# Optimization experiments

Measured on AMD Instinct MI355X. Metric: run time of the kernel, lower is better.

The kernel has to match this reference:

```python
import jax, jax.numpy as jnp
import numpy as np

N_NODES = 100000
N_EDGES = 1600000
IN_CH = 128
HIDDEN = 128


def setup_inputs() -> dict:
    key = jax.random.key(0)
    ks = jax.random.split(key, 8)
    def w(k, shape, fan_in):
        return jax.random.normal(k, shape, dtype=jnp.float32) * (1.0 / np.sqrt(fan_in))
    return {
        "x": jax.random.normal(ks[0], (N_NODES, IN_CH), dtype=jnp.float32),
        "edge_index": jax.random.randint(ks[1], (2, N_EDGES), 0, N_NODES, dtype=jnp.int32),
        # SAGEConv 1: lin_l (self, with bias), lin_r (neighbor mean, no bias)
        "Wl1": w(ks[2], (HIDDEN, IN_CH), IN_CH), "bl1": jnp.zeros((HIDDEN,), jnp.float32),
        "Wr1": w(ks[3], (HIDDEN, IN_CH), IN_CH),
        # SAGEConv 2
        "Wl2": w(ks[4], (HIDDEN, HIDDEN), HIDDEN), "bl2": jnp.zeros((HIDDEN,), jnp.float32),
        "Wr2": w(ks[5], (HIDDEN, HIDDEN), HIDDEN),
        # output head Linear(hidden, 1)
        "Wo": w(ks[6], (1, HIDDEN), HIDDEN), "bo": jnp.zeros((1,), jnp.float32),
    }


def _sage(x, src, dst, Wl, bl, Wr):
    # mean-aggregate source features onto destination nodes (PyG SAGEConv default)
    msg = x[src]                                             # [E, d] gather
    agg = jax.ops.segment_sum(msg, dst, num_segments=N_NODES)  # [N, d]
    cnt = jax.ops.segment_sum(jnp.ones((src.shape[0], 1), x.dtype), dst,
                              num_segments=N_NODES)            # [N, 1]
    mean = agg / jnp.maximum(cnt, 1.0)
    return x @ Wl.T + mean @ Wr.T + bl


def reference(x, edge_index, Wl1, bl1, Wr1, Wl2, bl2, Wr2, Wo, bo):
    src, dst = edge_index[0], edge_index[1]
    h = jax.nn.relu(_sage(x, src, dst, Wl1, bl1, Wr1))
    h = jax.nn.relu(_sage(h, src, dst, Wl2, bl2, Wr2))
    return (h @ Wo.T + bo).squeeze(-1)  # [N]
```

## Files before the change

### kernel.cpp

```cpp
#include <hip/hip_runtime.h>
#include <hip/hip_fp16.h>
#include <hip/hip_fp8.h>

#define N_NODES 100000
#define N_EDGES 1600000
#define C 128

#define NB_SHIFT 10
#define NB (1 << NB_SHIFT)
#define NBKT ((N_NODES + NB - 1) >> NB_SHIFT)
#define CAP 20480
#define CPT 4096
#define STG_BLOCKS ((N_EDGES + CPT - 1) / CPT)
#define CVB 782
#define PWB 32

typedef _Float16 half8 __attribute__((ext_vector_type(8)));
typedef float f32x4 __attribute__((ext_vector_type(4)));
typedef float f32x2 __attribute__((ext_vector_type(2)));

__device__ inline void fp8x4_to_f32(unsigned w, float* f) {
#if __has_builtin(__builtin_amdgcn_cvt_pk_f32_fp8)
    f32x2 lo = __builtin_amdgcn_cvt_pk_f32_fp8((int)w, false);
    f32x2 hi = __builtin_amdgcn_cvt_pk_f32_fp8((int)w, true);
    f[0] = lo[0]; f[1] = lo[1]; f[2] = hi[0]; f[3] = hi[1];
#else
    for (int i = 0; i < 4; i++) {
        __hip_fp8_e4m3 v;
        v.__x = (unsigned char)(w >> (8 * i));
        f[i] = (float)v;
    }
#endif
}

__device__ inline unsigned f32x4_to_fp8(float a, float b, float c, float d) {
#if __has_builtin(__builtin_amdgcn_cvt_pk_fp8_f32)
    int t = __builtin_amdgcn_cvt_pk_fp8_f32(a, b, 0, false);
    t = __builtin_amdgcn_cvt_pk_fp8_f32(c, d, t, true);
    return (unsigned)t;
#else
    __hip_fp8_e4m3 fa(a), fb(b), fc(c), fd(d);
    return (unsigned)fa.__x | ((unsigned)fb.__x << 8) | ((unsigned)fc.__x << 16) |
           ((unsigned)fd.__x << 24);
#endif
}

__device__ inline unsigned f32x2_to_fp8(float a, float b) {
#if __has_builtin(__builtin_amdgcn_cvt_pk_fp8_f32)
    return (unsigned)__builtin_amdgcn_cvt_pk_fp8_f32(a, b, 0, false);
#else
    __hip_fp8_e4m3 fa(a), fb(b);
    return (unsigned)fa.__x | ((unsigned)fb.__x << 8);
#endif
}


__global__ __launch_bounds__(512) void k_fusedA(
    const float* __restrict__ x, const int* __restrict__ src,
    const int* __restrict__ dst, const float* __restrict__ Wl1,
    const float* __restrict__ Wr1, const float* __restrict__ Wl2,
    const float* __restrict__ Wr2, int* __restrict__ gcur,
    uint2* __restrict__ S, __half* __restrict__ Xh, unsigned* __restrict__ X8u,
    __half* __restrict__ Wc1, __half* __restrict__ Wc2) {
    __shared__ int hist[128], sc[128], lstart[128], gbaseL[128];
    __shared__ uint2 stg[CPT];
    const int bid = blockIdx.x;
    const int t = threadIdx.x;

    if (bid < CVB) {
        const float4* xin = (const float4*)x;
        __half2* yout = (__half2*)Xh;
#pragma unroll
        for (int i = 0; i < 8; i++) {
            int idx = bid * 4096 + i * 512 + t;
            if (idx < N_NODES * C / 4) {
                float4 v = xin[idx];
                yout[idx * 2] = __floats2half2_rn(v.x, v.y);
                yout[idx * 2 + 1] = __floats2half2_rn(v.z, v.w);
                X8u[idx] = f32x4_to_fp8(v.x, v.y, v.z, v.w);
            }
        }
        return;
    }
    if (bid < CVB + PWB) {
        int i0 = ((bid - CVB) * 512 + t) * 4;
#pragma unroll
        for (int m = 0; m < 4; m++) {
            int i = i0 + m;
            if (i < 2 * 128 * 256) {
                int set = i >> 15;
                int j = i & 32767;
                int n_ = j >> 8, k = j & 255;
                const float* Wl = set ? Wl2 : Wl1;
                const float* Wr = set ? Wr2 : Wr1;
                float v = (k < 128) ? Wl[n_ * 128 + k] : Wr[n_ * 128 + (k - 128)];
                (set ? Wc2 : Wc1)[j] = __float2half_rn(v);
            }
        }
        return;
    }

    int base = (bid - CVB - PWB) * CPT;
    int cnt = N_EDGES - base;
    if (cnt > CPT) cnt = CPT;
    if (t < 128) hist[t] = 0;
    __syncthreads();
    unsigned s_[8], d_[8];
    int r_[8], b_[8];
#pragma unroll
    for (int i = 0; i < 8; i++) {
        int li = i * 512 + t;
        if (li < cnt) {
            int e = base + li;
            s_[i] = src[e];
            d_[i] = dst[e];
            b_[i] = d_[i] >> NB_SHIFT;
            r_[i] = atomicAdd(&hist[b_[i]], 1);
        } else {
            r_[i] = -1;
        }
    }
    __syncthreads();
    int hv = (t < 128) ? hist[t] : 0;
    if (t < 128) sc[t] = hv;
    __syncthreads();
    for (int off = 1; off < 128; off <<= 1) {
        int u = (t < 128 && t >= off) ? sc[t - off] : 0;
        __syncthreads();
        if (t < 128) sc[t] += u;
        __syncthreads();
    }
    if (t < 128) lstart[t] = sc[t] - hv;
    if (t < NBKT && hv) gbaseL[t] = t * CAP + atomicAdd(&gcur[t], hv);
    __syncthreads();
#pragma unroll
    for (int i = 0; i < 8; i++)
        if (r_[i] >= 0) stg[lstart[b_[i]] + r_[i]] = make_uint2(s_[i], d_[i]);
    __syncthreads();
    for (int slot = t; slot < cnt; slot += 512) {
        uint2 ed = stg[slot];
        int b = ed.y >> NB_SHIFT;
        S[gbaseL[b] + (slot - lstart[b])] = ed;
    }
}

__global__ __launch_bounds__(1024) void k_bfine(const uint2* __restrict__ S,
                                                const int* __restrict__ gcur,
                                                int* __restrict__ rowbeg,
                                                int* __restrict__ rowend,
                                                int* __restrict__ col) {
    __shared__ int hist[NB];
    __shared__ int wsum[16];
    int t = threadIdx.x, b = blockIdx.x;
    int nbeg = b << NB_SHIFT;
    int ebeg = b * CAP;
    int cnt = gcur[b];
    hist[t] = 0;
    __syncthreads();
    for (int e = t; e < cnt; e += 1024) atomicAdd(&hist[S[ebeg + e].y - nbeg], 1);
    __syncthreads();
    int v = hist[t];
    int inc = v;
    int lane = t & 63, wid = t >> 6;
#pragma unroll
    for (int off = 1; off < 64; off <<= 1) {
        int u = __shfl_up(inc, off);
        if (lane >= off) inc += u;
    }
    if (lane == 63) wsum[wid] = inc;
    __syncthreads();
    if (t < 16) {
        int wi = wsum[t];
#pragma unroll
        for (int off = 1; off < 16; off <<= 1) {
            int u = __shfl_up(wi, off);
            if (t >= off) wi += u;
        }
        wsum[t] = wi;
    }
    __syncthreads();
    int woff = (wid == 0) ? 0 : wsum[wid - 1];
    int excl = inc - v + woff;
    int g = nbeg + t;
    if (g < N_NODES) {
        rowbeg[g] = ebeg + excl;
        rowend[g] = ebeg + excl + v;
    }
    __syncthreads();
    hist[t] = excl;
    __syncthreads();
    for (int e = t; e < cnt; e += 1024) {
        uint2 ed = S[ebeg + e];
        int p = atomicAdd(&hist[ed.y - nbeg], 1);
        col[ebeg + p] = ed.x;
    }
}


__global__ __launch_bounds__(256) void k_mean_fp8(const unsigned char* __restrict__ X8,
                                                  __half* __restrict__ M,
                                                  const int* __restrict__ rowbeg,
                                                  const int* __restrict__ rowend,
                                                  const int* __restrict__ col) {
    int node = blockIdx.x * 32 + (threadIdx.x >> 3);
    if (node >= N_NODES) return;
    int seg = threadIdx.x & 7;
    int beg = rowbeg[node], end = rowend[node];
    float acc[16];
#pragma unroll
    for (int i = 0; i < 16; i++) acc[i] = 0.f;
    for (int e = beg; e < end; e += 8) {
        uint4 v[8];
        bool val[8];
#pragma unroll
        for (int u = 0; u < 8; u++) {
            int ee = e + u;
            val[u] = (ee < end);
            int s = col[val[u] ? ee : (end - 1)];
            v[u] = *(const uint4*)(X8 + (size_t)s * C + seg * 16);
        }
#pragma unroll
        for (int u = 0; u < 8; u++) {
            if (val[u]) {
                const unsigned* w = (const unsigned*)&v[u];
#pragma unroll
                for (int q = 0; q < 4; q++) {
                    float f[4];
                    fp8x4_to_f32(w[q], f);
                    acc[4 * q + 0] += f[0];
                    acc[4 * q + 1] += f[1];
                    acc[4 * q + 2] += f[2];
                    acc[4 * q + 3] += f[3];
                }
            }
        }
    }
    int deg = end - beg;
    float inv = 1.0f / (float)((deg > 0) ? deg : 1);
    __half2 o[8];
#pragma unroll
    for (int q = 0; q < 8; q++)
        o[q] = __floats2half2_rn(acc[2 * q] * inv, acc[2 * q + 1] * inv);
    uint4* dst0 = (uint4*)(M + (size_t)node * C + seg * 16);
    dst0[0] = ((uint4*)o)[0];
    dst0[1] = ((uint4*)o)[1];
}


template <int HEAD>
__global__ __launch_bounds__(256) void k_gemm2(
    const __half* __restrict__ A0, const __half* __restrict__ A1,
    const __half* __restrict__ W, const float* __restrict__ bias,
    __half* __restrict__ Hout, unsigned char* __restrict__ H8,
    const float* __restrict__ Wo, const float* __restrict__ bo,
    float* __restrict__ out) {
    __shared__ __half As[64][264];
    __shared__ float outs[4][64];
    const int tid = threadIdx.x;
    const int r0 = blockIdx.x * 64;

#pragma unroll
    for (int i = 0; i < 8; i++) {
        int s = tid + i * 256;
        int row = s >> 5, sg = s & 31;
        int gr = r0 + row;
        gr = (gr < N_NODES) ? gr : (N_NODES - 1);
        uint4 v;
        if (sg < 16)
            v = *(const uint4*)(A0 + (size_t)gr * C + sg * 8);
        else
            v = *(const uint4*)(A1 + (size_t)gr * C + (sg - 16) * 8);
        *(uint4*)&As[row][sg * 8] = v;
    }
    __syncthreads();

    const int wid = tid >> 6, lane = tid & 63;
    const int l15 = lane & 15, lk = lane >> 4;

    f32x4 acc[4][2];
#pragma unroll
    for (int m = 0; m < 4; m++)
#pragma unroll
        for (int n = 0; n < 2; n++) acc[m][n] = (f32x4)(0.0f);

#pragma unroll
    for (int c = 0; c < 8; c++) {
        half8 af[4], bf[2];
#pragma unroll
        for (int m = 0; m < 4; m++)
            af[m] = *(const half8*)&As[m * 16 + l15][c * 32 + lk * 8];
#pragma unroll
        for (int n = 0; n < 2; n++)
            bf[n] = *(const half8*)(W + (size_t)(wid * 32 + n * 16 + l15) * 256 +
                                    c * 32 + lk * 8);
#pragma unroll
        for (int m = 0; m < 4; m++)
#pragma unroll
            for (int n = 0; n < 2; n++)
                acc[m][n] =
                    __builtin_amdgcn_mfma_f32_16x16x32_f16(af[m], bf[n], acc[m][n], 0, 0, 0);
    }

    float bv[2];
#pragma unroll
    for (int n = 0; n < 2; n++) bv[n] = bias[wid * 32 + n * 16 + l15];
#pragma unroll
    for (int m = 0; m < 4; m++)
#pragma unroll
        for (int n = 0; n < 2; n++)
#pragma unroll
            for (int r = 0; r < 4; r++)
                acc[m][n][r] = fmaxf(acc[m][n][r] + bv[n], 0.f);

    if (!HEAD) {
#pragma unroll
        for (int m = 0; m < 4; m++) {
#pragma unroll
            for (int r = 0; r < 4; r++) {
                int row = r0 + m * 16 + lk * 4 + r;
                if (row < N_NODES) {
#pragma unroll
                    for (int n = 0; n < 2; n++)
                        Hout[(size_t)row * C + wid * 32 + n * 16 + l15] =
                            __float2half_rn(acc[m][n][r]);
                    unsigned t8 = f32x2_to_fp8(acc[m][0][r], acc[m][1][r]);
                    H8[(size_t)row * C + wid * 32 + l15] = (unsigned char)(t8 & 0xff);
                    H8[(size_t)row * C + wid * 32 + 16 + l15] =
                        (unsigned char)((t8 >> 8) & 0xff);
                }
            }
        }
    } else {
        float wv[2];
#pragma unroll
        for (int n = 0; n < 2; n++) wv[n] = Wo[wid * 32 + n * 16 + l15];
#pragma unroll
        for (int m = 0; m < 4; m++) {
#pragma unroll
            for (int r = 0; r < 4; r++) {
                float p = acc[m][0][r] * wv[0] + acc[m][1][r] * wv[1];
                p += __shfl_xor(p, 1);
                p += __shfl_xor(p, 2);
                p += __shfl_xor(p, 4);
                p += __shfl_xor(p, 8);
                if (l15 == 0) outs[wid][m * 16 + lk * 4 + r] = p;
            }
        }
        __syncthreads();
        if (tid < 64) {
            int row = r0 + tid;
            if (row < N_NODES)
                out[row] = outs[0][tid] + outs[1][tid] + outs[2][tid] + outs[3][tid] +
                           bo[0];
        }
    }
}


extern "C" void kernel_launch(void* const* d_in, const int* in_sizes, int n_in,
                              void* d_out, int out_size, void* d_ws, size_t ws_size,
                              hipStream_t stream) {
    const float* x   = (const float*)d_in[0];
    const int*   ei  = (const int*)d_in[1];
    const float* Wl1 = (const float*)d_in[2];
    const float* bl1 = (const float*)d_in[3];
    const float* Wr1 = (const float*)d_in[4];
    const float* Wl2 = (const float*)d_in[5];
    const float* bl2 = (const float*)d_in[6];
    const float* Wr2 = (const float*)d_in[7];
    const float* Wo  = (const float*)d_in[8];
    const float* bo  = (const float*)d_in[9];
    float* out = (float*)d_out;

    const int* src = ei;
    const int* dst = ei + N_EDGES;

    char* ws = (char*)d_ws;
    auto carve = [&](size_t bytes) {
        char* p = ws;
        ws += (bytes + 1023) & ~(size_t)1023;
        return p;
    };
    int*      gcur   = (int*)carve((size_t)NBKT * 4);
    int*      rowbeg = (int*)carve((size_t)N_NODES * 4);
    int*      rowend = (int*)carve((size_t)N_NODES * 4);
    int*      col    = (int*)carve((size_t)NBKT * CAP * 4);
    uint2*    S      = (uint2*)carve((size_t)NBKT * CAP * 8);
    __half*   Xh     = (__half*)carve((size_t)N_NODES * C * 2);
    __half*   Mh     = (__half*)carve((size_t)N_NODES * C * 2);
    __half*   Hh     = (__half*)carve((size_t)N_NODES * C * 2);
    unsigned char* X8 = (unsigned char*)carve((size_t)N_NODES * C);
    unsigned char* H8 = (unsigned char*)carve((size_t)N_NODES * C);
    __half*   Wc1    = (__half*)carve((size_t)128 * 256 * 2);
    __half*   Wc2    = (__half*)carve((size_t)128 * 256 * 2);

    hipMemsetAsync(gcur, 0, (size_t)NBKT * 4, stream);

    k_fusedA<<<CVB + PWB + STG_BLOCKS, 512, 0, stream>>>(
        x, src, dst, Wl1, Wr1, Wl2, Wr2, gcur, S, Xh, (unsigned*)X8, Wc1, Wc2);
    k_bfine<<<NBKT, 1024, 0, stream>>>(S, gcur, rowbeg, rowend, col);

    dim3 gM((N_NODES + 31) / 32), b256(256);
    dim3 gG((N_NODES + 63) / 64);

    k_mean_fp8<<<gM, b256, 0, stream>>>(X8, Mh, rowbeg, rowend, col);
    k_gemm2<0><<<gG, b256, 0, stream>>>(Xh, Mh, Wc1, bl1, Hh, H8, nullptr, nullptr,
                                        nullptr);
    k_mean_fp8<<<gM, b256, 0, stream>>>(H8, Mh, rowbeg, rowend, col);
    k_gemm2<1><<<gG, b256, 0, stream>>>(Hh, Mh, Wc2, bl2, nullptr, nullptr, Wo, bo,
                                        out);
}
```

Baseline: 172.4 us.

## Pack edge staging records into 32-bit words and predicate gathers in mean kernel

```diff
diff --git a/kernel.cpp b/kernel.cpp
--- a/kernel.cpp
+++ b/kernel.cpp
@@ -60,10 +60,10 @@
     const int* __restrict__ dst, const float* __restrict__ Wl1,
     const float* __restrict__ Wr1, const float* __restrict__ Wl2,
     const float* __restrict__ Wr2, int* __restrict__ gcur,
-    uint2* __restrict__ S, __half* __restrict__ Xh, unsigned* __restrict__ X8u,
+    unsigned* __restrict__ S, __half* __restrict__ Xh, unsigned* __restrict__ X8u,
     __half* __restrict__ Wc1, __half* __restrict__ Wc2) {
     __shared__ int hist[128], sc[128], lstart[128], gbaseL[128];
-    __shared__ uint2 stg[CPT];
+    __shared__ unsigned stg[CPT];
     const int bid = blockIdx.x;
     const int t = threadIdx.x;
 
@@ -135,16 +135,21 @@
     __syncthreads();
 #pragma unroll
     for (int i = 0; i < 8; i++)
-        if (r_[i] >= 0) stg[lstart[b_[i]] + r_[i]] = make_uint2(s_[i], d_[i]);
+        if (r_[i] >= 0)
+            stg[lstart[b_[i]] + r_[i]] = (s_[i] << NB_SHIFT) | (d_[i] & (NB - 1));
     __syncthreads();
     for (int slot = t; slot < cnt; slot += 512) {
-        uint2 ed = stg[slot];
-        int b = ed.y >> NB_SHIFT;
-        S[gbaseL[b] + (slot - lstart[b])] = ed;
-    }
-}
-
-__global__ __launch_bounds__(1024) void k_bfine(const uint2* __restrict__ S,
+        unsigned ed = stg[slot];
+        int lo = 0, hi = NBKT - 1;
+        while (lo < hi) {
+            int mid = (lo + hi + 1) >> 1;
+            if (lstart[mid] <= slot) lo = mid; else hi = mid - 1;
+        }
+        S[gbaseL[lo] + (slot - lstart[lo])] = ed;
+    }
+}
+
+__global__ __launch_bounds__(1024) void k_bfine(const unsigned* __restrict__ S,
                                                 const int* __restrict__ gcur,
                                                 int* __restrict__ rowbeg,
                                                 int* __restrict__ rowend,
@@ -157,7 +162,7 @@
     int cnt = gcur[b];
     hist[t] = 0;
     __syncthreads();
-    for (int e = t; e < cnt; e += 1024) atomicAdd(&hist[S[ebeg + e].y - nbeg], 1);
+    for (int e = t; e < cnt; e += 1024) atomicAdd(&hist[S[ebeg + e] & (NB - 1)], 1);
     __syncthreads();
     int v = hist[t];
     int inc = v;
@@ -190,9 +195,9 @@
     hist[t] = excl;
     __syncthreads();
     for (int e = t; e < cnt; e += 1024) {
-        uint2 ed = S[ebeg + e];
-        int p = atomicAdd(&hist[ed.y - nbeg], 1);
-        col[ebeg + p] = ed.x;
+        unsigned ed = S[ebeg + e];
+        int p = atomicAdd(&hist[ed & (NB - 1)], 1);
+        col[ebeg + p] = (int)(ed >> NB_SHIFT);
     }
 }
 
@@ -216,8 +221,10 @@
         for (int u = 0; u < 8; u++) {
             int ee = e + u;
             val[u] = (ee < end);
-            int s = col[val[u] ? ee : (end - 1)];
-            v[u] = *(const uint4*)(X8 + (size_t)s * C + seg * 16);
+            if (val[u]) {
+                int s = col[ee];
+                v[u] = *(const uint4*)(X8 + (size_t)s * C + seg * 16);
+            }
         }
 #pragma unroll
         for (int u = 0; u < 8; u++) {
@@ -385,7 +392,7 @@
     int*      rowbeg = (int*)carve((size_t)N_NODES * 4);
     int*      rowend = (int*)carve((size_t)N_NODES * 4);
     int*      col    = (int*)carve((size_t)NBKT * CAP * 4);
-    uint2*    S      = (uint2*)carve((size_t)NBKT * CAP * 8);
+    unsigned* S      = (unsigned*)carve((size_t)NBKT * CAP * 4);
     __half*   Xh     = (__half*)carve((size_t)N_NODES * C * 2);
     __half*   Mh     = (__half*)carve((size_t)N_NODES * C * 2);
     __half*   Hh     = (__half*)carve((size_t)N_NODES * C * 2);
```

New measurement: 182.5 us. 5.9% more time.
